# Kernel optimization log

Measured on AMD Instinct MI355X. Metric: run time of the kernel, lower is better.

The kernel has to match this reference:

```python
import jax, jax.numpy as jnp
import numpy as np

N = 4096
Q_DIM = K_DIM = V_DIM = OUT_DIM = ATTN_DIM = 512
NUM_HEADS = 8
HEAD_DIM = ATTN_DIM // NUM_HEADS
SCALE = float(HEAD_DIM) ** (-0.5)


def setup_inputs() -> dict:
    key = jax.random.key(0)
    ks = jax.random.split(key, 12)
    def lin(kw, kb, out_d, in_d):
        bound = 1.0 / np.sqrt(in_d)
        w = jax.random.uniform(kw, (out_d, in_d), jnp.float32, -bound, bound)
        b = jax.random.uniform(kb, (out_d,), jnp.float32, -bound, bound)
        return w, b
    wq_w, wq_b = lin(ks[0], ks[1], ATTN_DIM, Q_DIM)
    wk_w, wk_b = lin(ks[2], ks[3], ATTN_DIM, K_DIM)
    wv_w, wv_b = lin(ks[4], ks[5], ATTN_DIM, V_DIM)
    wo_w, wo_b = lin(ks[6], ks[7], OUT_DIM, ATTN_DIM)
    q = jax.random.normal(ks[8], (N, Q_DIM), jnp.float32)
    k = jax.random.normal(ks[9], (N, K_DIM), jnp.float32)
    v = jax.random.normal(ks[10], (N, V_DIM), jnp.float32)
    mask = jax.random.uniform(ks[11], (N, N)) < 0.1  # True = masked out
    return {"q": q, "k": k, "v": v, "mask": mask,
            "wq_w": wq_w, "wq_b": wq_b, "wk_w": wk_w, "wk_b": wk_b,
            "wv_w": wv_w, "wv_b": wv_b, "wo_w": wo_w, "wo_b": wo_b}


def reference(q, k, v, mask, wq_w, wq_b, wk_w, wk_b, wv_w, wv_b, wo_w, wo_b):
    # Linear projections (torch Linear: x @ W.T + b)
    qp = q @ wq_w.T + wq_b  # (N, A)
    kp = k @ wk_w.T + wk_b
    vp = v @ wv_w.T + wv_b
    # (N, A) -> (H, N, dh)
    qh = qp.reshape(N, NUM_HEADS, HEAD_DIM).transpose(1, 0, 2)
    kh = kp.reshape(N, NUM_HEADS, HEAD_DIM).transpose(1, 0, 2)
    vh = vp.reshape(N, NUM_HEADS, HEAD_DIM).transpose(1, 0, 2)
    attn = jnp.einsum('hnd,hmd->hnm', qh, kh) * SCALE  # (H, N, N)
    attn = jnp.where(mask[None, :, :], jnp.float32(-1e6), attn)
    attn = jax.nn.softmax(attn, axis=-1)
    o = jnp.einsum('hnm,hmd->hnd', attn, vh)  # (H, N, dh)
    o = o.transpose(1, 0, 2).reshape(N, ATTN_DIM)
    return o @ wo_w.T + wo_b  # (N, out_dim)
```

## Files before the change

### kernel.cpp

```cpp
#include <hip/hip_runtime.h>


typedef __attribute__((ext_vector_type(8))) short bf16x8;
typedef __attribute__((ext_vector_type(4))) float f32x4;

#define N_TOK 4096
#define QSCALE 0.18033688f

__device__ __forceinline__ unsigned short f2bf(float f) {
  unsigned u = __float_as_uint(f);
  return (unsigned short)((u + 0x7FFFu + ((u >> 16) & 1u)) >> 16);
}
__device__ __forceinline__ unsigned pack_bf16(float a, float b) {
  unsigned ua = __float_as_uint(a), ub = __float_as_uint(b);
  ua += 0x7FFFu + ((ua >> 16) & 1u);
  ub += 0x7FFFu + ((ub >> 16) & 1u);
  return (ua >> 16) | (ub & 0xFFFF0000u);
}
__device__ __forceinline__ f32x4 mfma16(bf16x8 a, bf16x8 b, f32x4 c) {
  return __builtin_amdgcn_mfma_f32_16x16x32_bf16(a, b, c, 0, 0, 0);
}
__device__ __forceinline__ float fast_exp2(float x) {
#if __has_builtin(__builtin_amdgcn_exp2f)
  return __builtin_amdgcn_exp2f(x);
#else
  return exp2f(x);
#endif
}

__global__ __launch_bounds__(256) void detect_kernel(
    const unsigned* __restrict__ mask, unsigned* __restrict__ flags) {
  __shared__ int s_bad;
  int t = threadIdx.x;
  if (t == 0) s_bad = 0;
  __syncthreads();
  if (mask[t] > 1u) atomicOr(&s_bad, 1);
  __syncthreads();
  if (t == 0) {
    flags[0] = 0;
    flags[1] = s_bad ? 1u : 0u;
  }
}

__global__ __launch_bounds__(256) void pack_mask_kernel(
    const void* __restrict__ m, unsigned long long* __restrict__ bitsT,
    const unsigned* __restrict__ flags) {
  int gt = blockIdx.x * 256 + threadIdx.x;
  int wave = gt >> 6;
  int lane = threadIdx.x & 63;
  int row = wave >> 4;
  int sub = wave & 15;
  int base = wave * 256;
  unsigned long long b0, b1, b2, b3;
  if (flags[1]) {
    const unsigned char* m8 = (const unsigned char*)m;
    b0 = __ballot(m8[base + 0 * 64 + lane] != 0);
    b1 = __ballot(m8[base + 1 * 64 + lane] != 0);
    b2 = __ballot(m8[base + 2 * 64 + lane] != 0);
    b3 = __ballot(m8[base + 3 * 64 + lane] != 0);
  } else {
    const int* m4 = (const int*)m;
    b0 = __ballot(m4[base + 0 * 64 + lane] != 0);
    b1 = __ballot(m4[base + 1 * 64 + lane] != 0);
    b2 = __ballot(m4[base + 2 * 64 + lane] != 0);
    b3 = __ballot(m4[base + 3 * 64 + lane] != 0);
  }
  if (lane < 4) {
    unsigned long long bl = lane == 0 ? b0 : lane == 1 ? b1 : lane == 2 ? b2 : b3;
    bitsT[(size_t)(sub * 4 + lane) * N_TOK + row] = bl;
  }
}

__global__ __launch_bounds__(256) void convert_kernel(
    const float* __restrict__ s0, const float* __restrict__ s1,
    const float* __restrict__ s2, const float* __restrict__ s3,
    const float* __restrict__ s4, const float* __restrict__ s5,
    const float* __restrict__ s6, unsigned short* __restrict__ d0,
    unsigned short* __restrict__ d1, unsigned short* __restrict__ d2,
    unsigned short* __restrict__ d3, unsigned short* __restrict__ d4,
    unsigned short* __restrict__ d5, unsigned short* __restrict__ d6) {
  int z = blockIdx.y;
  int nblk = (z < 3) ? 1024 : 128;
  if (blockIdx.x >= nblk) return;
  const float* src = z == 0 ? s0 : z == 1 ? s1 : z == 2 ? s2 : z == 3 ? s3
                     : z == 4 ? s4 : z == 5 ? s5 : s6;
  unsigned short* dst = z == 0 ? d0 : z == 1 ? d1 : z == 2 ? d2 : z == 3 ? d3
                        : z == 4 ? d4 : z == 5 ? d5 : d6;
  int idx = (blockIdx.x * 256 + threadIdx.x) * 8;
  float4 f0 = *(const float4*)(src + idx);
  float4 f1 = *(const float4*)(src + idx + 4);
  uint4 o;
  o.x = pack_bf16(f0.x, f0.y);
  o.y = pack_bf16(f0.z, f0.w);
  o.z = pack_bf16(f1.x, f1.y);
  o.w = pack_bf16(f1.z, f1.w);
  *(uint4*)(dst + idx) = o;
}

template <int O32, int TRANS>
__device__ __forceinline__ void gemm_body(
    const unsigned short* __restrict__ A, const unsigned short* __restrict__ W,
    const float* __restrict__ bias, void* __restrict__ out, float oscale) {
  __shared__ unsigned short As[128 * 72];
  __shared__ unsigned short Bs[128 * 72];
  const int t = threadIdx.x;
  const int lane = t & 63, w = t >> 6;
  const int wm = w & 1, wn = w >> 1;
  const int q4 = lane >> 4, i15 = lane & 15;
  const int m0 = blockIdx.y * 128, n0 = blockIdx.x * 128;
  f32x4 acc[4][4] = {};
  const int sr = t >> 2;
  const int sc = (t & 3) * 16;
  for (int k0 = 0; k0 < 512; k0 += 64) {
    __syncthreads();
#pragma unroll
    for (int p = 0; p < 2; ++p) {
      int row = sr + p * 64;
      const unsigned short* pa = A + (size_t)(m0 + row) * 512 + k0 + sc;
      const unsigned short* pb = W + (size_t)(n0 + row) * 512 + k0 + sc;
      uint4 a0 = *(const uint4*)pa, a1 = *(const uint4*)(pa + 8);
      uint4 b0 = *(const uint4*)pb, b1 = *(const uint4*)(pb + 8);
      *(uint4*)(As + row * 72 + sc) = a0;
      *(uint4*)(As + row * 72 + sc + 8) = a1;
      *(uint4*)(Bs + row * 72 + sc) = b0;
      *(uint4*)(Bs + row * 72 + sc + 8) = b1;
    }
    __syncthreads();
#pragma unroll
    for (int ks = 0; ks < 2; ++ks) {
      bf16x8 af[4], bfr[4];
#pragma unroll
      for (int mt = 0; mt < 4; ++mt)
        af[mt] = *(const bf16x8*)(As + (wm * 64 + mt * 16 + i15) * 72 + q4 * 8 + ks * 32);
#pragma unroll
      for (int nt = 0; nt < 4; ++nt)
        bfr[nt] = *(const bf16x8*)(Bs + (wn * 64 + nt * 16 + i15) * 72 + q4 * 8 + ks * 32);
#pragma unroll
      for (int mt = 0; mt < 4; ++mt)
#pragma unroll
        for (int nt = 0; nt < 4; ++nt)
          acc[mt][nt] = mfma16(af[mt], bfr[nt], acc[mt][nt]);
    }
  }
#pragma unroll
  for (int nt = 0; nt < 4; ++nt) {
    int col = n0 + wn * 64 + nt * 16 + i15;
    float bv = bias[col];
    if (TRANS) {
      unsigned short* ob_ = (unsigned short*)out +
                            (size_t)(col >> 6) * (64 * N_TOK) +
                            (size_t)(col & 63) * N_TOK;
#pragma unroll
      for (int mt = 0; mt < 4; ++mt) {
        int rowb = m0 + wm * 64 + mt * 16 + q4 * 4;
        uint2 pr;
        pr.x = pack_bf16(acc[mt][nt][0] + bv, acc[mt][nt][1] + bv);
        pr.y = pack_bf16(acc[mt][nt][2] + bv, acc[mt][nt][3] + bv);
        *(uint2*)(ob_ + rowb) = pr;
      }
    } else {
#pragma unroll
      for (int mt = 0; mt < 4; ++mt) {
        int rowb = m0 + wm * 64 + mt * 16 + q4 * 4;
#pragma unroll
        for (int rr = 0; rr < 4; ++rr) {
          int idx = (rowb + rr) * 512 + col;
          float val = (acc[mt][nt][rr] + bv) * oscale;
          if (O32) ((float*)out)[idx] = val;
          else ((unsigned short*)out)[idx] = f2bf(val);
        }
      }
    }
  }
}

__global__ __launch_bounds__(256) void qkv_gemm_kernel(
    const unsigned short* __restrict__ qc, const unsigned short* __restrict__ kc,
    const unsigned short* __restrict__ vc, const unsigned short* __restrict__ wqc,
    const unsigned short* __restrict__ wkc, const unsigned short* __restrict__ wvc,
    const float* __restrict__ bq, const float* __restrict__ bk,
    const float* __restrict__ bv, unsigned short* __restrict__ outbase) {
  int z = blockIdx.z;
  if (z == 0) {
    gemm_body<0, 0>(qc, wqc, bq, outbase, QSCALE);
  } else if (z == 1) {
    gemm_body<0, 0>(kc, wkc, bk, outbase + (size_t)N_TOK * 512, 1.0f);
  } else {
    gemm_body<0, 1>(vc, wvc, bv, outbase + 2ull * N_TOK * 512, 1.0f);
  }
}

__global__ __launch_bounds__(256) void out_gemm_kernel(
    const unsigned short* __restrict__ A, const unsigned short* __restrict__ W,
    const float* __restrict__ B, float* __restrict__ out) {
  gemm_body<1, 0>(A, W, B, out, 1.0f);
}

__global__ __launch_bounds__(256, 2) void attn_kernel(
    const unsigned short* __restrict__ qp, const unsigned short* __restrict__ kp,
    const unsigned short* __restrict__ vpT,
    const unsigned long long* __restrict__ mbT,
    float* __restrict__ Op, float* __restrict__ dp) {
  __shared__ unsigned short Ks[2][64 * 64];
  __shared__ unsigned short Vt[2][64 * 64];
  const int t = threadIdx.x;
  const int l = t & 63, w = t >> 6;
  const int q4 = l >> 4, i15 = l & 15;
  const int iblk = blockIdx.x * 256;
  const int head = blockIdx.y;
  const int chunk = blockIdx.z;
  const int ch = head * 64;
  const int i0 = iblk + w * 64;
  const int ji = l >> 3;
  const int sg = l & 7;
  const int r0 = w * 2;
  const int j0base = chunk * 1024;
  bf16x8 qf[4][2];
#pragma unroll
  for (int nt = 0; nt < 4; ++nt) {
    const unsigned short* qr = qp + (size_t)(i0 + nt * 16 + i15) * 512 + ch;
#pragma unroll
    for (int ks = 0; ks < 2; ++ks)
      qf[nt][ks] = *(const bf16x8*)(qr + ks * 32 + q4 * 8);
  }
  f32x4 oacc[4][4] = {};
  float den[4] = {0.f, 0.f, 0.f, 0.f};
  const unsigned short* vbase = vpT + (size_t)head * (64 * N_TOK);
  uint4 kst[2], vst[2];
  unsigned long long mwc[4], mwn[4];
#pragma unroll
  for (int rr = 0; rr < 2; ++rr) {
    int row = (r0 + rr) * 8 + ji;
    kst[rr] = *(const uint4*)(kp + (size_t)(j0base + row) * 512 + ch + sg * 8);
    vst[rr] = *(const uint4*)(vbase + (size_t)row * N_TOK + j0base + sg * 8);
  }
#pragma unroll
  for (int nt = 0; nt < 4; ++nt)
    mwc[nt] = mbT[(size_t)(chunk * 16 + 0) * N_TOK + i0 + nt * 16 + i15];
  for (int jt = 0; jt < 16; ++jt) {
    unsigned short* KsB = Ks[jt & 1];
    unsigned short* VtB = Vt[jt & 1];
#pragma unroll
    for (int rr = 0; rr < 2; ++rr) {
      int r = r0 + rr;
      int row = r * 8 + ji;
      *(uint4*)(KsB + row * 64 + ((sg ^ ji ^ r) * 8)) = kst[rr];
      const unsigned* vs = (const unsigned*)&vst[rr];
#pragma unroll
      for (int c2 = 0; c2 < 2; ++c2) {
        int kg = (sg >> 2) * 4 + (sg & 1) * 2 + c2;
        int hh = (sg >> 1) & 1;
        *(uint2*)(VtB + row * 64 + ((kg ^ ji ^ r) * 8) + hh * 4) =
            make_uint2(vs[c2 * 2], vs[c2 * 2 + 1]);
      }
    }
    __syncthreads();
    {
      int jn = (jt + 1) & 15;
#pragma unroll
      for (int nt = 0; nt < 4; ++nt)
        mwn[nt] = mbT[(size_t)(chunk * 16 + jn) * N_TOK + i0 + nt * 16 + i15];
      int jng = j0base + jn * 64;
#pragma unroll
      for (int rr = 0; rr < 2; ++rr) {
        int row = (r0 + rr) * 8 + ji;
        kst[rr] = *(const uint4*)(kp + (size_t)(jng + row) * 512 + ch + sg * 8);
        vst[rr] = *(const uint4*)(vbase + (size_t)row * N_TOK + jng + sg * 8);
      }
    }
    unsigned pk[4][8];
#pragma unroll
    for (int mtj = 0; mtj < 4; ++mtj) {
      int js = mtj * 16 + i15;
      bf16x8 Kf0 =
          *(const bf16x8*)(KsB + js * 64 + (((0 * 4 + q4) ^ (js & 7) ^ (js >> 3)) * 8));
      bf16x8 Kf1 =
          *(const bf16x8*)(KsB + js * 64 + (((1 * 4 + q4) ^ (js & 7) ^ (js >> 3)) * 8));
#pragma unroll
      for (int nt = 0; nt < 4; ++nt) {
        f32x4 s = {0.f, 0.f, 0.f, 0.f};
        s = mfma16(Kf0, qf[nt][0], s);
        s = mfma16(Kf1, qf[nt][1], s);
        unsigned nib = (unsigned)(mwc[nt] >> (mtj * 16 + q4 * 4)) & 15u;
        float p0 = fast_exp2((nib & 1u) ? -200.f : s[0]);
        float p1 = fast_exp2((nib & 2u) ? -200.f : s[1]);
        float p2 = fast_exp2((nib & 4u) ? -200.f : s[2]);
        float p3 = fast_exp2((nib & 8u) ? -200.f : s[3]);
        den[nt] += (p0 + p1) + (p2 + p3);
        pk[nt][mtj * 2] = pack_bf16(p0, p1);
        pk[nt][mtj * 2 + 1] = pack_bf16(p2, p3);
      }
    }
#pragma unroll
    for (int ks = 0; ks < 2; ++ks) {
      bf16x8 Vf[4];
#pragma unroll
      for (int mtd = 0; mtd < 4; ++mtd) {
        int d = mtd * 16 + i15;
        int kg = ks * 4 + q4;
        Vf[mtd] =
            *(const bf16x8*)(VtB + d * 64 + ((kg ^ (d & 7) ^ (d >> 3)) * 8));
      }
#pragma unroll
      for (int nt = 0; nt < 4; ++nt) {
        union { unsigned u[4]; bf16x8 v; } pf;
        pf.u[0] = pk[nt][ks * 4 + 0];
        pf.u[1] = pk[nt][ks * 4 + 1];
        pf.u[2] = pk[nt][ks * 4 + 2];
        pf.u[3] = pk[nt][ks * 4 + 3];
#pragma unroll
        for (int mtd = 0; mtd < 4; ++mtd)
          oacc[mtd][nt] = mfma16(Vf[mtd], pf.v, oacc[mtd][nt]);
      }
    }
#pragma unroll
    for (int nt = 0; nt < 4; ++nt) mwc[nt] = mwn[nt];
  }
  float* Opc = Op + ((size_t)(chunk * 8 + head) * N_TOK) * 64;
#pragma unroll
  for (int nt = 0; nt < 4; ++nt) {
    float dn = den[nt];
    dn += __shfl_xor(dn, 16);
    dn += __shfl_xor(dn, 32);
    int row = i0 + nt * 16 + i15;
#pragma unroll
    for (int mtd = 0; mtd < 4; ++mtd)
      *(f32x4*)(Opc + (size_t)row * 64 + mtd * 16 + q4 * 4) = oacc[mtd][nt];
    if (q4 == 0) dp[(size_t)(chunk * 8 + head) * N_TOK + row] = dn;
  }
}

__global__ __launch_bounds__(256) void reduce_kernel(
    const float* __restrict__ Op, const float* __restrict__ dp,
    unsigned short* __restrict__ ob) {
  int x = blockIdx.x * 256 + threadIdx.x;
  int i = x >> 7;
  int c = (x & 127) * 4;
  int h = c >> 6;
  int d = c & 63;
  const size_t CH = (size_t)8 * N_TOK * 64;
  size_t base = ((size_t)h * N_TOK + i) * 64 + d;
  float4 a0 = *(const float4*)(Op + base);
  float4 a1 = *(const float4*)(Op + CH + base);
  float4 a2 = *(const float4*)(Op + 2 * CH + base);
  float4 a3 = *(const float4*)(Op + 3 * CH + base);
  float den = dp[(size_t)h * N_TOK + i] + dp[(size_t)(8 + h) * N_TOK + i] +
              dp[(size_t)(16 + h) * N_TOK + i] + dp[(size_t)(24 + h) * N_TOK + i];
  float inv = 1.0f / den;
  float sx = (a0.x + a1.x + a2.x + a3.x) * inv;
  float sy = (a0.y + a1.y + a2.y + a3.y) * inv;
  float sz = (a0.z + a1.z + a2.z + a3.z) * inv;
  float sw = (a0.w + a1.w + a2.w + a3.w) * inv;
  uint2 o;
  o.x = pack_bf16(sx, sy);
  o.y = pack_bf16(sz, sw);
  *(uint2*)(ob + (size_t)i * 512 + c) = o;
}

extern "C" void kernel_launch(void* const* d_in, const int* in_sizes, int n_in,
                              void* d_out, int out_size, void* d_ws, size_t ws_size,
                              hipStream_t stream) {
  const float* q = (const float*)d_in[0];
  const float* k = (const float*)d_in[1];
  const float* v = (const float*)d_in[2];
  const void* mask = d_in[3];
  const float* wq = (const float*)d_in[4];
  const float* bq = (const float*)d_in[5];
  const float* wk = (const float*)d_in[6];
  const float* bk = (const float*)d_in[7];
  const float* wv = (const float*)d_in[8];
  const float* bv = (const float*)d_in[9];
  const float* wo = (const float*)d_in[10];
  const float* bo = (const float*)d_in[11];

  char* ws = (char*)d_ws;
  const size_t MB = 1ull << 20;
  unsigned* flags = (unsigned*)ws;
  unsigned short* woc = (unsigned short*)(ws + 4096);
  unsigned long long* mbT = (unsigned long long*)(ws + 1 * MB);
  unsigned short* qkvp = (unsigned short*)(ws + 3 * MB);
  unsigned short* ob = (unsigned short*)(ws + 15 * MB);
  unsigned short* qc = (unsigned short*)(ws + 19 * MB);
  unsigned short* kc = (unsigned short*)(ws + 23 * MB);
  unsigned short* vc = (unsigned short*)(ws + 27 * MB);
  unsigned short* wqc = (unsigned short*)(ws + 31 * MB);
  unsigned short* wkc = (unsigned short*)(ws + 31 * MB + 512 * 1024);
  unsigned short* wvc = (unsigned short*)(ws + 32 * MB);
  float* Op = (float*)(ws + 19 * MB);
  float* dp = (float*)(ws + 51 * MB);

  detect_kernel<<<1, 256, 0, stream>>>((const unsigned*)mask, flags);
  pack_mask_kernel<<<16384, 256, 0, stream>>>(mask, mbT, flags);
  convert_kernel<<<dim3(1024, 7), 256, 0, stream>>>(
      q, k, v, wq, wk, wv, wo, qc, kc, vc, wqc, wkc, wvc, woc);
  qkv_gemm_kernel<<<dim3(4, 32, 3), 256, 0, stream>>>(qc, kc, vc, wqc, wkc,
                                                      wvc, bq, bk, bv, qkvp);
  attn_kernel<<<dim3(16, 8, 4), 256, 0, stream>>>(
      qkvp, qkvp + (size_t)N_TOK * 512, qkvp + 2ull * N_TOK * 512, mbT, Op, dp);
  reduce_kernel<<<2048, 256, 0, stream>>>(Op, dp, ob);
  out_gemm_kernel<<<dim3(4, 32), 256, 0, stream>>>(ob, woc, bo, (float*)d_out);
}
```

Before: 244.6 us.

## Shrink GEMM N-tile, unroll attention loop by two, drop mask-format detection

```diff
diff --git a/kernel.cpp b/kernel.cpp
--- a/kernel.cpp
+++ b/kernel.cpp
@@ -28,43 +28,18 @@
 #endif
 }
 
-__global__ __launch_bounds__(256) void detect_kernel(
-    const unsigned* __restrict__ mask, unsigned* __restrict__ flags) {
-  __shared__ int s_bad;
-  int t = threadIdx.x;
-  if (t == 0) s_bad = 0;
-  __syncthreads();
-  if (mask[t] > 1u) atomicOr(&s_bad, 1);
-  __syncthreads();
-  if (t == 0) {
-    flags[0] = 0;
-    flags[1] = s_bad ? 1u : 0u;
-  }
-}
-
 __global__ __launch_bounds__(256) void pack_mask_kernel(
-    const void* __restrict__ m, unsigned long long* __restrict__ bitsT,
-    const unsigned* __restrict__ flags) {
+    const int* __restrict__ m, unsigned long long* __restrict__ bitsT) {
   int gt = blockIdx.x * 256 + threadIdx.x;
   int wave = gt >> 6;
   int lane = threadIdx.x & 63;
   int row = wave >> 4;
   int sub = wave & 15;
   int base = wave * 256;
-  unsigned long long b0, b1, b2, b3;
-  if (flags[1]) {
-    const unsigned char* m8 = (const unsigned char*)m;
-    b0 = __ballot(m8[base + 0 * 64 + lane] != 0);
-    b1 = __ballot(m8[base + 1 * 64 + lane] != 0);
-    b2 = __ballot(m8[base + 2 * 64 + lane] != 0);
-    b3 = __ballot(m8[base + 3 * 64 + lane] != 0);
-  } else {
-    const int* m4 = (const int*)m;
-    b0 = __ballot(m4[base + 0 * 64 + lane] != 0);
-    b1 = __ballot(m4[base + 1 * 64 + lane] != 0);
-    b2 = __ballot(m4[base + 2 * 64 + lane] != 0);
-    b3 = __ballot(m4[base + 3 * 64 + lane] != 0);
-  }
+  unsigned long long b0 = __ballot(m[base + 0 * 64 + lane] != 0);
+  unsigned long long b1 = __ballot(m[base + 1 * 64 + lane] != 0);
+  unsigned long long b2 = __ballot(m[base + 2 * 64 + lane] != 0);
+  unsigned long long b3 = __ballot(m[base + 3 * 64 + lane] != 0);
   if (lane < 4) {
     unsigned long long bl = lane == 0 ? b0 : lane == 1 ? b1 : lane == 2 ? b2 : b3;
     bitsT[(size_t)(sub * 4 + lane) * N_TOK + row] = bl;
@@ -98,17 +73,17 @@
 }
 
 template <int O32, int TRANS>
-__device__ __forceinline__ void gemm_body(
+__device__ __forceinline__ void gemm_body64(
     const unsigned short* __restrict__ A, const unsigned short* __restrict__ W,
     const float* __restrict__ bias, void* __restrict__ out, float oscale) {
   __shared__ unsigned short As[128 * 72];
-  __shared__ unsigned short Bs[128 * 72];
+  __shared__ unsigned short Bs[64 * 72];
   const int t = threadIdx.x;
   const int lane = t & 63, w = t >> 6;
   const int wm = w & 1, wn = w >> 1;
   const int q4 = lane >> 4, i15 = lane & 15;
-  const int m0 = blockIdx.y * 128, n0 = blockIdx.x * 128;
-  f32x4 acc[4][4] = {};
+  const int m0 = blockIdx.y * 128, n0 = blockIdx.x * 64;
+  f32x4 acc[4][2] = {};
   const int sr = t >> 2;
   const int sc = (t & 3) * 16;
   for (int k0 = 0; k0 < 512; k0 += 64) {
@@ -117,34 +92,36 @@
     for (int p = 0; p < 2; ++p) {
       int row = sr + p * 64;
       const unsigned short* pa = A + (size_t)(m0 + row) * 512 + k0 + sc;
-      const unsigned short* pb = W + (size_t)(n0 + row) * 512 + k0 + sc;
       uint4 a0 = *(const uint4*)pa, a1 = *(const uint4*)(pa + 8);
-      uint4 b0 = *(const uint4*)pb, b1 = *(const uint4*)(pb + 8);
       *(uint4*)(As + row * 72 + sc) = a0;
       *(uint4*)(As + row * 72 + sc + 8) = a1;
-      *(uint4*)(Bs + row * 72 + sc) = b0;
-      *(uint4*)(Bs + row * 72 + sc + 8) = b1;
+    }
+    {
+      const unsigned short* pb = W + (size_t)(n0 + sr) * 512 + k0 + sc;
+      uint4 b0 = *(const uint4*)pb, b1 = *(const uint4*)(pb + 8);
+      *(uint4*)(Bs + sr * 72 + sc) = b0;
+      *(uint4*)(Bs + sr * 72 + sc + 8) = b1;
     }
     __syncthreads();
 #pragma unroll
     for (int ks = 0; ks < 2; ++ks) {
-      bf16x8 af[4], bfr[4];
+      bf16x8 af[4], bfr[2];
 #pragma unroll
       for (int mt = 0; mt < 4; ++mt)
         af[mt] = *(const bf16x8*)(As + (wm * 64 + mt * 16 + i15) * 72 + q4 * 8 + ks * 32);
 #pragma unroll
-      for (int nt = 0; nt < 4; ++nt)
-        bfr[nt] = *(const bf16x8*)(Bs + (wn * 64 + nt * 16 + i15) * 72 + q4 * 8 + ks * 32);
+      for (int nt = 0; nt < 2; ++nt)
+        bfr[nt] = *(const bf16x8*)(Bs + (wn * 32 + nt * 16 + i15) * 72 + q4 * 8 + ks * 32);
 #pragma unroll
       for (int mt = 0; mt < 4; ++mt)
 #pragma unroll
-        for (int nt = 0; nt < 4; ++nt)
+        for (int nt = 0; nt < 2; ++nt)
           acc[mt][nt] = mfma16(af[mt], bfr[nt], acc[mt][nt]);
     }
   }
 #pragma unroll
-  for (int nt = 0; nt < 4; ++nt) {
-    int col = n0 + wn * 64 + nt * 16 + i15;
+  for (int nt = 0; nt < 2; ++nt) {
+    int col = n0 + wn * 32 + nt * 16 + i15;
     float bv = bias[col];
     if (TRANS) {
       unsigned short* ob_ = (unsigned short*)out +
@@ -182,19 +159,84 @@
     const float* __restrict__ bv, unsigned short* __restrict__ outbase) {
   int z = blockIdx.z;
   if (z == 0) {
-    gemm_body<0, 0>(qc, wqc, bq, outbase, QSCALE);
+    gemm_body64<0, 0>(qc, wqc, bq, outbase, QSCALE);
   } else if (z == 1) {
-    gemm_body<0, 0>(kc, wkc, bk, outbase + (size_t)N_TOK * 512, 1.0f);
+    gemm_body64<0, 0>(kc, wkc, bk, outbase + (size_t)N_TOK * 512, 1.0f);
   } else {
-    gemm_body<0, 1>(vc, wvc, bv, outbase + 2ull * N_TOK * 512, 1.0f);
+    gemm_body64<0, 1>(vc, wvc, bv, outbase + 2ull * N_TOK * 512, 1.0f);
   }
 }
 
 __global__ __launch_bounds__(256) void out_gemm_kernel(
     const unsigned short* __restrict__ A, const unsigned short* __restrict__ W,
     const float* __restrict__ B, float* __restrict__ out) {
-  gemm_body<1, 0>(A, W, B, out, 1.0f);
-}
+  gemm_body64<1, 0>(A, W, B, out, 1.0f);
+}
+
+#define ATTN_BODY(BUF, MWIN, MWOUT)                                           \
+  do {                                                                        \
+    char* KsB = (char*)(Ks[BUF]);                                             \
+    char* VtB = (char*)(Vt[BUF]);                                             \
+    *(uint4*)(KsB + ksto0) = kst0;                                            \
+    *(uint4*)(KsB + ksto1) = kst1;                                            \
+    {                                                                         \
+      const unsigned* vs = (const unsigned*)&vst0;                            \
+      *(uint2*)(VtB + vsto00) = make_uint2(vs[0], vs[1]);                     \
+      *(uint2*)(VtB + vsto01) = make_uint2(vs[2], vs[3]);                     \
+    }                                                                         \
+    {                                                                         \
+      const unsigned* vs = (const unsigned*)&vst1;                            \
+      *(uint2*)(VtB + vsto10) = make_uint2(vs[0], vs[1]);                     \
+      *(uint2*)(VtB + vsto11) = make_uint2(vs[2], vs[3]);                     \
+    }                                                                         \
+    __syncthreads();                                                          \
+    kst0 = *(const uint4*)(kgp);                                              \
+    kst1 = *(const uint4*)(kgp + 8192);                                       \
+    vst0 = *(const uint4*)(vgp);                                              \
+    vst1 = *(const uint4*)(vgp + 65536);                                      \
+    MWOUT[0] = *(const unsigned long long*)(mgp);                             \
+    MWOUT[1] = *(const unsigned long long*)(mgp + 128);                       \
+    MWOUT[2] = *(const unsigned long long*)(mgp + 256);                       \
+    MWOUT[3] = *(const unsigned long long*)(mgp + 384);                       \
+    kgp += 65536;                                                             \
+    vgp += 128;                                                               \
+    mgp += 32768;                                                             \
+    unsigned pk[4][8];                                                        \
+    _Pragma("unroll") for (int mtj = 0; mtj < 4; ++mtj) {                     \
+      bf16x8 Kf0 = *(const bf16x8*)(KsB + kfo[mtj][0]);                       \
+      bf16x8 Kf1 = *(const bf16x8*)(KsB + kfo[mtj][1]);                       \
+      _Pragma("unroll") for (int nt = 0; nt < 4; ++nt) {                      \
+        f32x4 s = {0.f, 0.f, 0.f, 0.f};                                       \
+        s = mfma16(Kf0, qf[nt][0], s);                                        \
+        s = mfma16(Kf1, qf[nt][1], s);                                        \
+        unsigned nib = (unsigned)(MWIN[nt] >> (mtj * 16 + q4 * 4)) & 15u;     \
+        float p0 = fast_exp2((nib & 1u) ? -200.f : s[0]);                     \
+        float p1 = fast_exp2((nib & 2u) ? -200.f : s[1]);                     \
+        float p2 = fast_exp2((nib & 4u) ? -200.f : s[2]);                     \
+        float p3 = fast_exp2((nib & 8u) ? -200.f : s[3]);                     \
+        den[nt] += (p0 + p1) + (p2 + p3);                                     \
+        pk[nt][mtj * 2] = pack_bf16(p0, p1);                                  \
+        pk[nt][mtj * 2 + 1] = pack_bf16(p2, p3);                              \
+      }                                                                       \
+    }                                                                         \
+    _Pragma("unroll") for (int ks = 0; ks < 2; ++ks) {                        \
+      bf16x8 Vf[4];                                                           \
+      _Pragma("unroll") for (int mtd = 0; mtd < 4; ++mtd) Vf[mtd] =           \
+          *(const bf16x8*)(VtB + vfo[ks][mtd]);                               \
+      _Pragma("unroll") for (int nt = 0; nt < 4; ++nt) {                      \
+        union {                                                               \
+          unsigned u[4];                                                      \
+          bf16x8 v;                                                           \
+        } pf;                                                                 \
+        pf.u[0] = pk[nt][ks * 4 + 0];                                         \
+        pf.u[1] = pk[nt][ks * 4 + 1];                                         \
+        pf.u[2] = pk[nt][ks * 4 + 2];                                         \
+        pf.u[3] = pk[nt][ks * 4 + 3];                                         \
+        _Pragma("unroll") for (int mtd = 0; mtd < 4; ++mtd) oacc[mtd][nt] =   \
+            mfma16(Vf[mtd], pf.v, oacc[mtd][nt]);                             \
+      }                                                                       \
+    }                                                                         \
+  } while (0)
 
 __global__ __launch_bounds__(256, 2) void attn_kernel(
     const unsigned short* __restrict__ qp, const unsigned short* __restrict__ kp,
@@ -225,96 +267,58 @@
   }
   f32x4 oacc[4][4] = {};
   float den[4] = {0.f, 0.f, 0.f, 0.f};
-  const unsigned short* vbase = vpT + (size_t)head * (64 * N_TOK);
-  uint4 kst[2], vst[2];
+  int kfo[4][2], vfo[2][4];
+#pragma unroll
+  for (int mtj = 0; mtj < 4; ++mtj) {
+    int js = mtj * 16 + i15;
+    int h = (js & 7) ^ (js >> 3);
+#pragma unroll
+    for (int ksd = 0; ksd < 2; ++ksd)
+      kfo[mtj][ksd] = (js * 64 + (((ksd * 4 + q4) ^ h) * 8)) * 2;
+  }
+#pragma unroll
+  for (int ks = 0; ks < 2; ++ks)
+#pragma unroll
+    for (int mtd = 0; mtd < 4; ++mtd) {
+      int d = mtd * 16 + i15;
+      int h = (d & 7) ^ (d >> 3);
+      vfo[ks][mtd] = (d * 64 + (((ks * 4 + q4) ^ h) * 8)) * 2;
+    }
+  int ksto0, ksto1, vsto00, vsto01, vsto10, vsto11;
+  {
+    int r = r0, row = r * 8 + ji;
+    ksto0 = (row * 64 + ((sg ^ ji ^ r) * 8)) * 2;
+    int hh = (sg >> 1) & 1;
+    int kg0 = (sg >> 2) * 4 + (sg & 1) * 2;
+    vsto00 = (row * 64 + ((kg0 ^ ji ^ r) * 8) + hh * 4) * 2;
+    vsto01 = (row * 64 + (((kg0 + 1) ^ ji ^ r) * 8) + hh * 4) * 2;
+    r = r0 + 1; row = r * 8 + ji;
+    ksto1 = (row * 64 + ((sg ^ ji ^ r) * 8)) * 2;
+    vsto10 = (row * 64 + ((kg0 ^ ji ^ r) * 8) + hh * 4) * 2;
+    vsto11 = (row * 64 + (((kg0 + 1) ^ ji ^ r) * 8) + hh * 4) * 2;
+  }
+  const char* kgp =
+      (const char*)kp + ((size_t)(j0base + r0 * 8 + ji) * 512 + ch + sg * 8) * 2;
+  const char* vgp = (const char*)(vpT + (size_t)head * 64 * N_TOK) +
+                    ((size_t)(r0 * 8 + ji) * N_TOK + j0base + sg * 8) * 2;
+  const char* mgp =
+      (const char*)mbT + ((size_t)(chunk * 16) * N_TOK + i0 + i15) * 8;
+  uint4 kst0, kst1, vst0, vst1;
   unsigned long long mwc[4], mwn[4];
-#pragma unroll
-  for (int rr = 0; rr < 2; ++rr) {
-    int row = (r0 + rr) * 8 + ji;
-    kst[rr] = *(const uint4*)(kp + (size_t)(j0base + row) * 512 + ch + sg * 8);
-    vst[rr] = *(const uint4*)(vbase + (size_t)row * N_TOK + j0base + sg * 8);
-  }
-#pragma unroll
-  for (int nt = 0; nt < 4; ++nt)
-    mwc[nt] = mbT[(size_t)(chunk * 16 + 0) * N_TOK + i0 + nt * 16 + i15];
-  for (int jt = 0; jt < 16; ++jt) {
-    unsigned short* KsB = Ks[jt & 1];
-    unsigned short* VtB = Vt[jt & 1];
-#pragma unroll
-    for (int rr = 0; rr < 2; ++rr) {
-      int r = r0 + rr;
-      int row = r * 8 + ji;
-      *(uint4*)(KsB + row * 64 + ((sg ^ ji ^ r) * 8)) = kst[rr];
-      const unsigned* vs = (const unsigned*)&vst[rr];
-#pragma unroll
-      for (int c2 = 0; c2 < 2; ++c2) {
-        int kg = (sg >> 2) * 4 + (sg & 1) * 2 + c2;
-        int hh = (sg >> 1) & 1;
-        *(uint2*)(VtB + row * 64 + ((kg ^ ji ^ r) * 8) + hh * 4) =
-            make_uint2(vs[c2 * 2], vs[c2 * 2 + 1]);
-      }
-    }
-    __syncthreads();
-    {
-      int jn = (jt + 1) & 15;
-#pragma unroll
-      for (int nt = 0; nt < 4; ++nt)
-        mwn[nt] = mbT[(size_t)(chunk * 16 + jn) * N_TOK + i0 + nt * 16 + i15];
-      int jng = j0base + jn * 64;
-#pragma unroll
-      for (int rr = 0; rr < 2; ++rr) {
-        int row = (r0 + rr) * 8 + ji;
-        kst[rr] = *(const uint4*)(kp + (size_t)(jng + row) * 512 + ch + sg * 8);
-        vst[rr] = *(const uint4*)(vbase + (size_t)row * N_TOK + jng + sg * 8);
-      }
-    }
-    unsigned pk[4][8];
-#pragma unroll
-    for (int mtj = 0; mtj < 4; ++mtj) {
-      int js = mtj * 16 + i15;
-      bf16x8 Kf0 =
-          *(const bf16x8*)(KsB + js * 64 + (((0 * 4 + q4) ^ (js & 7) ^ (js >> 3)) * 8));
-      bf16x8 Kf1 =
-          *(const bf16x8*)(KsB + js * 64 + (((1 * 4 + q4) ^ (js & 7) ^ (js >> 3)) * 8));
-#pragma unroll
-      for (int nt = 0; nt < 4; ++nt) {
-        f32x4 s = {0.f, 0.f, 0.f, 0.f};
-        s = mfma16(Kf0, qf[nt][0], s);
-        s = mfma16(Kf1, qf[nt][1], s);
-        unsigned nib = (unsigned)(mwc[nt] >> (mtj * 16 + q4 * 4)) & 15u;
-        float p0 = fast_exp2((nib & 1u) ? -200.f : s[0]);
-        float p1 = fast_exp2((nib & 2u) ? -200.f : s[1]);
-        float p2 = fast_exp2((nib & 4u) ? -200.f : s[2]);
-        float p3 = fast_exp2((nib & 8u) ? -200.f : s[3]);
-        den[nt] += (p0 + p1) + (p2 + p3);
-        pk[nt][mtj * 2] = pack_bf16(p0, p1);
-        pk[nt][mtj * 2 + 1] = pack_bf16(p2, p3);
-      }
-    }
-#pragma unroll
-    for (int ks = 0; ks < 2; ++ks) {
-      bf16x8 Vf[4];
-#pragma unroll
-      for (int mtd = 0; mtd < 4; ++mtd) {
-        int d = mtd * 16 + i15;
-        int kg = ks * 4 + q4;
-        Vf[mtd] =
-            *(const bf16x8*)(VtB + d * 64 + ((kg ^ (d & 7) ^ (d >> 3)) * 8));
-      }
-#pragma unroll
-      for (int nt = 0; nt < 4; ++nt) {
-        union { unsigned u[4]; bf16x8 v; } pf;
-        pf.u[0] = pk[nt][ks * 4 + 0];
-        pf.u[1] = pk[nt][ks * 4 + 1];
-        pf.u[2] = pk[nt][ks * 4 + 2];
-        pf.u[3] = pk[nt][ks * 4 + 3];
-#pragma unroll
-        for (int mtd = 0; mtd < 4; ++mtd)
-          oacc[mtd][nt] = mfma16(Vf[mtd], pf.v, oacc[mtd][nt]);
-      }
-    }
-#pragma unroll
-    for (int nt = 0; nt < 4; ++nt) mwc[nt] = mwn[nt];
+  kst0 = *(const uint4*)(kgp);
+  kst1 = *(const uint4*)(kgp + 8192);
+  vst0 = *(const uint4*)(vgp);
+  vst1 = *(const uint4*)(vgp + 65536);
+  mwc[0] = *(const unsigned long long*)(mgp);
+  mwc[1] = *(const unsigned long long*)(mgp + 128);
+  mwc[2] = *(const unsigned long long*)(mgp + 256);
+  mwc[3] = *(const unsigned long long*)(mgp + 384);
+  kgp += 65536;
+  vgp += 128;
+  mgp += 32768;
+  for (int jp = 0; jp < 8; ++jp) {
+    ATTN_BODY(0, mwc, mwn);
+    ATTN_BODY(1, mwn, mwc);
   }
   float* Opc = Op + ((size_t)(chunk * 8 + head) * N_TOK) * 64;
 #pragma unroll
@@ -363,7 +367,7 @@
   const float* q = (const float*)d_in[0];
   const float* k = (const float*)d_in[1];
   const float* v = (const float*)d_in[2];
-  const void* mask = d_in[3];
+  const int* mask = (const int*)d_in[3];
   const float* wq = (const float*)d_in[4];
   const float* bq = (const float*)d_in[5];
   const float* wk = (const float*)d_in[6];
@@ -375,7 +379,6 @@
 
   char* ws = (char*)d_ws;
   const size_t MB = 1ull << 20;
-  unsigned* flags = (unsigned*)ws;
   unsigned short* woc = (unsigned short*)(ws + 4096);
   unsigned long long* mbT = (unsigned long long*)(ws + 1 * MB);
   unsigned short* qkvp = (unsigned short*)(ws + 3 * MB);
@@ -389,14 +392,13 @@
   float* Op = (float*)(ws + 19 * MB);
   float* dp = (float*)(ws + 51 * MB);
 
-  detect_kernel<<<1, 256, 0, stream>>>((const unsigned*)mask, flags);
-  pack_mask_kernel<<<16384, 256, 0, stream>>>(mask, mbT, flags);
+  pack_mask_kernel<<<16384, 256, 0, stream>>>(mask, mbT);
   convert_kernel<<<dim3(1024, 7), 256, 0, stream>>>(
       q, k, v, wq, wk, wv, wo, qc, kc, vc, wqc, wkc, wvc, woc);
-  qkv_gemm_kernel<<<dim3(4, 32, 3), 256, 0, stream>>>(qc, kc, vc, wqc, wkc,
+  qkv_gemm_kernel<<<dim3(8, 32, 3), 256, 0, stream>>>(qc, kc, vc, wqc, wkc,
                                                       wvc, bq, bk, bv, qkvp);
   attn_kernel<<<dim3(16, 8, 4), 256, 0, stream>>>(
       qkvp, qkvp + (size_t)N_TOK * 512, qkvp + 2ull * N_TOK * 512, mbT, Op, dp);
   reduce_kernel<<<2048, 256, 0, stream>>>(Op, dp, ob);
-  out_gemm_kernel<<<dim3(4, 32), 256, 0, stream>>>(ob, woc, bo, (float*)d_out);
-}
+  out_gemm_kernel<<<dim3(8, 32), 256, 0, stream>>>(ob, woc, bo, (float*)d_out);
+}
```

Measured after the change: 244.2 us. Within noise of the previous version (-0.2%).
